# Kernel tuning notes

Hardware: AMD Instinct MI355X
Metric: run time of the kernel (lower is better)

The kernel has to match this reference:

```python
import jax, jax.numpy as jnp
import numpy as np

BATCH = 2048
N = 2 * BATCH
TEMP = 0.5
BN_EPS = 1e-5
COS_EPS = 1e-8

# Precompute (constant) flat indices of the negative entries: all (i,j) with
# j != i and j != i +- BATCH. Each row has exactly N-2 negatives.
_mask = np.ones((N, N), dtype=bool)
np.fill_diagonal(_mask, False)
for _i in range(BATCH):
    _mask[_i, BATCH + _i] = False
    _mask[BATCH + _i, _i] = False
NEG_IDX = np.nonzero(_mask.reshape(-1))[0]  # (N*(N-2),)


def _projector(h, W1, gamma, beta, W2, b2):
    # Linear (no bias) -> BatchNorm1d (training-mode batch stats) -> ReLU -> Linear
    x = h @ W1.T                                   # (B, latent)
    mu = jnp.mean(x, axis=0)
    var = jnp.mean(jnp.square(x - mu), axis=0)     # biased var, as torch BN
    x = (x - mu) * jax.lax.rsqrt(var + BN_EPS) * gamma + beta
    x = jax.nn.relu(x)
    return x @ W2.T + b2                           # (B, proj)


def setup_inputs() -> dict:
    key = jax.random.key(0)
    ks = jax.random.split(key, 4)
    latent, proj = 2048, 256
    return {
        "h_i": jax.random.normal(ks[0], (BATCH, latent), jnp.float32),
        "h_j": jax.random.normal(ks[1], (BATCH, latent), jnp.float32),
        "W1": jax.random.normal(ks[2], (latent, latent), jnp.float32) / np.sqrt(latent),
        "gamma": jnp.ones((latent,), jnp.float32),
        "beta": jnp.zeros((latent,), jnp.float32),
        "W2": jax.random.normal(ks[3], (proj, latent), jnp.float32) / np.sqrt(latent),
        "b2": jnp.zeros((proj,), jnp.float32),
    }


def reference(h_i, h_j, W1, gamma, beta, W2, b2):
    z_i = _projector(h_i, W1, gamma, beta, W2, b2)
    z_j = _projector(h_j, W1, gamma, beta, W2, b2)
    z = jnp.concatenate([z_i, z_j], axis=0)                      # (N, proj)
    # cosine similarity: normalize once, then a single GEMM
    zn = z / jnp.maximum(jnp.linalg.norm(z, axis=1, keepdims=True), COS_EPS)
    sim = (zn @ zn.T) / TEMP                                     # (N, N)
    sim_i_j = jnp.diagonal(sim, offset=BATCH)                    # (BATCH,)
    sim_j_i = jnp.diagonal(sim, offset=-BATCH)                   # (BATCH,)
    positives = jnp.concatenate([sim_i_j, sim_j_i])[:, None]     # (N, 1)
    negatives = sim.reshape(-1)[NEG_IDX].reshape(N, N - 2)       # (N, N-2)
    logits = jnp.concatenate([positives, negatives], axis=1)     # (N, N-1)
    # cross-entropy with label 0 for every row, reduction='sum', then / N
    loss = jnp.sum(jax.nn.logsumexp(logits, axis=1) - logits[:, 0]) / N
    return loss
```

## Files before the change

kernel.cpp:

```cpp
#include <hip/hip_runtime.h>
#include <math.h>

#define BATCH   2048
#define NROWS   4096
#define LATENT  2048
#define PROJ    256
#define TEMP_INV 2.0f
#define BN_EPS  1e-5f
#define COS_EPS 1e-8f

typedef __bf16 bf16x8 __attribute__((ext_vector_type(8)));
typedef float  f32x4  __attribute__((ext_vector_type(4)));

__device__ __forceinline__ unsigned short f2bf(float f) {
    union { float f; unsigned int u; } c; c.f = f;
    return (unsigned short)((c.u + 0x7FFFu + ((c.u >> 16) & 1u)) >> 16);
}
__device__ __forceinline__ float bf2f(unsigned short h) {
    union { unsigned int u; float f; } c; c.u = ((unsigned int)h) << 16;
    return c.f;
}

__device__ __forceinline__ void gl_lds16(const unsigned short* g, unsigned short* l) {
    __builtin_amdgcn_global_load_lds(
        (__attribute__((address_space(1))) void*)g,
        (__attribute__((address_space(3))) void*)l, 16, 0, 0);
}

#define G1 1048576
#define G2 2097152
#define G3 3145728
#define G4 3276800
__global__ __launch_bounds__(256) void cvt_all_kernel(
    const float* __restrict__ h_i, const float* __restrict__ h_j,
    const float* __restrict__ W1,  const float* __restrict__ W2,
    unsigned short* __restrict__ dst)
{
    int i = blockIdx.x * 256 + threadIdx.x;
    if (i >= G4) return;
    const float* src; int off;
    if (i < G1)      { src = h_i; off = i; }
    else if (i < G2) { src = h_j; off = i - G1; }
    else if (i < G3) { src = W1;  off = i - G2; }
    else             { src = W2;  off = i - G3; }
    float4 v = reinterpret_cast<const float4*>(src)[off];
    ushort4 o;
    o.x = f2bf(v.x); o.y = f2bf(v.y); o.z = f2bf(v.z); o.w = f2bf(v.w);
    reinterpret_cast<ushort4*>(dst)[i] = o;
}

template<int KSTRIDE, int KLEN, int WM, int WN>
__device__ __forceinline__ void mfma_loop(
    const unsigned short* __restrict__ Ab,
    const unsigned short* __restrict__ Bb,
    unsigned short* As, unsigned short* Bs,
    f32x4 acc[WM][WN], int tid)
{
    constexpr int BM = WM * 32;
    constexpr int BN = WN * 32;
    const int wid = tid >> 6, lane = tid & 63;
    const int mblk = (wid >> 1) * (WM * 16);
    const int nblk = (wid & 1) * (WN * 16);
    const int lr = lane & 15, lk = lane >> 4;
    for (int k0 = 0; k0 < KLEN; k0 += 32) {
        __syncthreads();
        #pragma unroll
        for (int u = 0; u < BM / 64; ++u) {
            int li = u * 256 + tid;
            gl_lds16(Ab + (size_t)(li >> 2) * KSTRIDE + k0 + (li & 3) * 8, As + li * 8);
        }
        #pragma unroll
        for (int u = 0; u < BN / 64; ++u) {
            int li = u * 256 + tid;
            gl_lds16(Bb + (size_t)(li >> 2) * KSTRIDE + k0 + (li & 3) * 8, Bs + li * 8);
        }
        __syncthreads();
        bf16x8 af[WM], bv[WN];
        #pragma unroll
        for (int i = 0; i < WM; ++i)
            af[i] = *reinterpret_cast<const bf16x8*>(As + (mblk + i * 16 + lr) * 32 + lk * 8);
        #pragma unroll
        for (int j = 0; j < WN; ++j)
            bv[j] = *reinterpret_cast<const bf16x8*>(Bs + (nblk + j * 16 + lr) * 32 + lk * 8);
        #pragma unroll
        for (int i = 0; i < WM; ++i)
            #pragma unroll
            for (int j = 0; j < WN; ++j)
                acc[i][j] = __builtin_amdgcn_mfma_f32_16x16x32_bf16(af[i], bv[j], acc[i][j], 0, 0, 0);
    }
}

__global__ __launch_bounds__(256) void gemm1_mfma(
    const unsigned short* __restrict__ Hb, const unsigned short* __restrict__ W1b,
    unsigned short* __restrict__ Xb, float* __restrict__ sums, float* __restrict__ sumsqs)
{
    __shared__ __align__(16) unsigned short As[64 * 32];
    __shared__ __align__(16) unsigned short Bs[128 * 32];
    const int tid = threadIdx.x;
    const int m0 = blockIdx.y * 64, n0 = blockIdx.x * 128;
    f32x4 zero = {0.f, 0.f, 0.f, 0.f};
    f32x4 acc[2][4];
    #pragma unroll
    for (int i = 0; i < 2; ++i)
        #pragma unroll
        for (int j = 0; j < 4; ++j) acc[i][j] = zero;
    mfma_loop<LATENT, LATENT, 2, 4>(Hb + (size_t)m0 * LATENT, W1b + (size_t)n0 * LATENT,
                                    As, Bs, acc, tid);
    const int wid = tid >> 6, lane = tid & 63;
    const int mblk = (wid >> 1) * 32, nblk = (wid & 1) * 64;
    const int lr = lane & 15, lq = lane >> 4;
    const int half = m0 >> 11;
    #pragma unroll
    for (int j = 0; j < 4; ++j) {
        float s = 0.f, q = 0.f;
        #pragma unroll
        for (int i = 0; i < 2; ++i)
            #pragma unroll
            for (int r = 0; r < 4; ++r) {
                float v = acc[i][j][r];
                s += v; q += v * v;
                int row = m0 + mblk + i * 16 + lq * 4 + r;
                int col = n0 + nblk + j * 16 + lr;
                Xb[(size_t)row * LATENT + col] = f2bf(v);
            }
        s += __shfl_xor(s, 16, 64);  q += __shfl_xor(q, 16, 64);
        s += __shfl_xor(s, 32, 64);  q += __shfl_xor(q, 32, 64);
        if (lq == 0) {
            int col = n0 + nblk + j * 16 + lr;
            atomicAdd(&sums[half * LATENT + col], s);
            atomicAdd(&sumsqs[half * LATENT + col], q);
        }
    }
}

__global__ __launch_bounds__(256) void bn_final_kernel(
    const float* __restrict__ sums, const float* __restrict__ sumsqs,
    const float* __restrict__ gamma, const float* __restrict__ beta,
    float* __restrict__ scaleA, float* __restrict__ shiftA)
{
    const int idx = blockIdx.x * 256 + threadIdx.x;
    const int c = idx & (LATENT - 1);
    float mu  = sums[idx] * (1.0f / BATCH);
    float var = sumsqs[idx] * (1.0f / BATCH) - mu * mu;
    float inv = rsqrtf(var + BN_EPS);
    float sc = gamma[c] * inv;
    scaleA[idx] = sc;
    shiftA[idx] = beta[c] - mu * sc;
}

__global__ __launch_bounds__(256) void bnrelu_kernel(
    unsigned short* __restrict__ Xb, const float* __restrict__ scaleA,
    const float* __restrict__ shiftA)
{
    int idx = (blockIdx.x * 256 + threadIdx.x) * 8;
    int row = idx >> 11;
    int col = idx & (LATENT - 1);
    int half = row >> 11;
    ushort4 a = *reinterpret_cast<const ushort4*>(Xb + idx);
    ushort4 b = *reinterpret_cast<const ushort4*>(Xb + idx + 4);
    float4 s0 = *reinterpret_cast<const float4*>(scaleA + half * LATENT + col);
    float4 s1 = *reinterpret_cast<const float4*>(scaleA + half * LATENT + col + 4);
    float4 h0 = *reinterpret_cast<const float4*>(shiftA + half * LATENT + col);
    float4 h1 = *reinterpret_cast<const float4*>(shiftA + half * LATENT + col + 4);
    ushort4 oa, ob;
    oa.x = f2bf(fmaxf(fmaf(bf2f(a.x), s0.x, h0.x), 0.f));
    oa.y = f2bf(fmaxf(fmaf(bf2f(a.y), s0.y, h0.y), 0.f));
    oa.z = f2bf(fmaxf(fmaf(bf2f(a.z), s0.z, h0.z), 0.f));
    oa.w = f2bf(fmaxf(fmaf(bf2f(a.w), s0.w, h0.w), 0.f));
    ob.x = f2bf(fmaxf(fmaf(bf2f(b.x), s1.x, h1.x), 0.f));
    ob.y = f2bf(fmaxf(fmaf(bf2f(b.y), s1.y, h1.y), 0.f));
    ob.z = f2bf(fmaxf(fmaf(bf2f(b.z), s1.z, h1.z), 0.f));
    ob.w = f2bf(fmaxf(fmaf(bf2f(b.w), s1.w, h1.w), 0.f));
    *reinterpret_cast<ushort4*>(Xb + idx) = oa;
    *reinterpret_cast<ushort4*>(Xb + idx + 4) = ob;
}

__global__ __launch_bounds__(256) void gemm2_mfma(
    const unsigned short* __restrict__ Xb, const unsigned short* __restrict__ W2b,
    float* __restrict__ Zp)
{
    __shared__ __align__(16) unsigned short As[128 * 32];
    __shared__ __align__(16) unsigned short Bs[64 * 32];
    const int tid = threadIdx.x;
    const int m0 = blockIdx.y * 128, n0 = blockIdx.x * 64, kc = blockIdx.z;
    f32x4 zero = {0.f, 0.f, 0.f, 0.f};
    f32x4 acc[4][2];
    #pragma unroll
    for (int i = 0; i < 4; ++i) { acc[i][0] = zero; acc[i][1] = zero; }
    mfma_loop<LATENT, 512, 4, 2>(Xb + (size_t)m0 * LATENT + kc * 512,
                                 W2b + (size_t)n0 * LATENT + kc * 512, As, Bs, acc, tid);
    float* Zk = Zp + (size_t)kc * NROWS * PROJ;
    const int wid = tid >> 6, lane = tid & 63;
    const int mblk = (wid >> 1) * 64, nblk = (wid & 1) * 32;
    const int lr = lane & 15, lq = lane >> 4;
    #pragma unroll
    for (int i = 0; i < 4; ++i)
        #pragma unroll
        for (int j = 0; j < 2; ++j)
            #pragma unroll
            for (int r = 0; r < 4; ++r) {
                int row = m0 + mblk + i * 16 + lq * 4 + r;
                int col = n0 + nblk + j * 16 + lr;
                Zk[(size_t)row * PROJ + col] = acc[i][j][r];
            }
}

__global__ __launch_bounds__(256) void rownorm_kernel(
    const float* __restrict__ Zp, const float* __restrict__ b2,
    unsigned short* __restrict__ ZNb)
{
    const int wave = threadIdx.x >> 6;
    const int lane = threadIdx.x & 63;
    const int row = blockIdx.x * 4 + wave;
    float v[4];
    float sq = 0.f;
    #pragma unroll
    for (int i = 0; i < 4; ++i) {
        int col = lane + i * 64;
        float t = b2[col];
        #pragma unroll
        for (int c = 0; c < 4; ++c)
            t += Zp[(size_t)c * NROWS * PROJ + (size_t)row * PROJ + col];
        v[i] = t;
        sq += t * t;
    }
    #pragma unroll
    for (int off = 32; off > 0; off >>= 1) sq += __shfl_xor(sq, off, 64);
    float inv = 1.0f / fmaxf(sqrtf(sq), COS_EPS);
    #pragma unroll
    for (int i = 0; i < 4; ++i)
        ZNb[(size_t)row * PROJ + lane + i * 64] = f2bf(v[i] * inv);
}

__global__ __launch_bounds__(256) void simlse_mfma(
    const unsigned short* __restrict__ ZNb, float* __restrict__ rowsum,
    float* __restrict__ dgA, float* __restrict__ posA)
{
    __shared__ __align__(16) unsigned short As[128 * 32];
    __shared__ __align__(16) unsigned short Bs[128 * 32];
    const int tid = threadIdx.x;
    const int r0 = blockIdx.y * 128, j0 = blockIdx.x * 128;
    f32x4 zero = {0.f, 0.f, 0.f, 0.f};
    f32x4 acc[4][4];
    #pragma unroll
    for (int i = 0; i < 4; ++i)
        #pragma unroll
        for (int j = 0; j < 4; ++j) acc[i][j] = zero;
    mfma_loop<PROJ, PROJ, 4, 4>(ZNb + (size_t)r0 * PROJ, ZNb + (size_t)j0 * PROJ,
                                As, Bs, acc, tid);
    const int wid = tid >> 6, lane = tid & 63;
    const int mblk = (wid >> 1) * 64, nblk = (wid & 1) * 64;
    const int lr = lane & 15, lq = lane >> 4;
    #pragma unroll
    for (int i = 0; i < 4; ++i)
        #pragma unroll
        for (int r = 0; r < 4; ++r) {
            int R = r0 + mblk + i * 16 + lq * 4 + r;
            int P = (R < BATCH) ? R + BATCH : R - BATCH;
            float t = 0.f;
            #pragma unroll
            for (int j = 0; j < 4; ++j) {
                int J = j0 + nblk + j * 16 + lr;
                float s = acc[i][j][r] * TEMP_INV;
                float e = __expf(s);
                t += e;
                if (J == R) dgA[R] = e;
                if (J == P) posA[R] = s;
            }
            t += __shfl_xor(t, 1, 64);
            t += __shfl_xor(t, 2, 64);
            t += __shfl_xor(t, 4, 64);
            t += __shfl_xor(t, 8, 64);
            if (lr == 0) atomicAdd(&rowsum[R], t);
        }
}

__global__ __launch_bounds__(256) void loss_kernel(
    const float* __restrict__ rowsum, const float* __restrict__ dgA,
    const float* __restrict__ posA, float* __restrict__ out)
{
    __shared__ float red[256];
    float s = 0.f;
    for (int r = threadIdx.x; r < NROWS; r += 256)
        s += logf(rowsum[r] - dgA[r]) - posA[r];
    red[threadIdx.x] = s;
    __syncthreads();
    for (int off = 128; off > 0; off >>= 1) {
        if (threadIdx.x < off) red[threadIdx.x] += red[threadIdx.x + off];
        __syncthreads();
    }
    if (threadIdx.x == 0) out[0] = red[0] * (1.0f / NROWS);
}

extern "C" void kernel_launch(void* const* d_in, const int* in_sizes, int n_in,
                              void* d_out, int out_size, void* d_ws, size_t ws_size,
                              hipStream_t stream)
{
    const float* h_i   = (const float*)d_in[0];
    const float* h_j   = (const float*)d_in[1];
    const float* W1    = (const float*)d_in[2];
    const float* gamma = (const float*)d_in[3];
    const float* beta  = (const float*)d_in[4];
    const float* W2    = (const float*)d_in[5];
    const float* b2    = (const float*)d_in[6];
    float* out = (float*)d_out;

    float* Zp     = (float*)d_ws;
    float* sums   = Zp + (size_t)4 * NROWS * PROJ;
    float* sumsqs = sums + 2 * LATENT;
    float* rowsum = sumsqs + 2 * LATENT;
    float* scaleA = rowsum + NROWS;
    float* shiftA = scaleA + 2 * LATENT;
    float* dgA    = shiftA + 2 * LATENT;
    float* posA   = dgA + NROWS;
    unsigned short* Hb  = (unsigned short*)(posA + NROWS);
    unsigned short* W1b = Hb + (size_t)NROWS * LATENT;
    unsigned short* W2b = W1b + (size_t)LATENT * LATENT;
    unsigned short* Xb  = W2b + (size_t)PROJ * LATENT;
    unsigned short* ZNb = Xb + (size_t)NROWS * LATENT;

    hipMemsetAsync(sums, 0, (size_t)(4 * LATENT + NROWS) * sizeof(float), stream);

    cvt_all_kernel<<<(G4 + 255) / 256, 256, 0, stream>>>(h_i, h_j, W1, W2, Hb);
    gemm1_mfma<<<dim3(LATENT / 128, NROWS / 64), 256, 0, stream>>>(Hb, W1b, Xb, sums, sumsqs);
    bn_final_kernel<<<(2 * LATENT) / 256, 256, 0, stream>>>(sums, sumsqs, gamma, beta, scaleA, shiftA);
    bnrelu_kernel<<<(NROWS * LATENT / 8) / 256, 256, 0, stream>>>(Xb, scaleA, shiftA);
    gemm2_mfma<<<dim3(PROJ / 64, NROWS / 128, 4), 256, 0, stream>>>(Xb, W2b, Zp);
    rownorm_kernel<<<NROWS / 4, 256, 0, stream>>>(Zp, b2, ZNb);
    simlse_mfma<<<dim3(NROWS / 128, NROWS / 128), 256, 0, stream>>>(ZNb, rowsum, dgA, posA);
    loss_kernel<<<1, 256, 0, stream>>>(rowsum, dgA, posA, out);
}
```

Before: 212.7 us.

## Use FP8 GEMM1, fuse BN+ReLU into GEMM2, swizzle LDS tiles

Inputs h and W1 are now quantized to FP8 e4m3, with W1 pre-scaled by 32. GEMM1 runs on fp8 MFMA with 128x128 tiles and a K-step of 128, and rescales the result in the epilogue. The standalone BN+ReLU pass is removed: GEMM2 applies scale, shift and ReLU to the A fragments after they come out of LDS. LDS layouts are also XOR-swizzled to cut bank conflicts. The main aim is to halve GEMM1 operand bytes and raise MFMA throughput, at the cost of FP8 quantization error in the projector's first layer.

Result: faster. 191.0 us (-10.2%).

```diff
diff --git a/kernel.cpp b/kernel.cpp
--- a/kernel.cpp
+++ b/kernel.cpp
@@ -1,4 +1,5 @@
 #include <hip/hip_runtime.h>
+#include <hip/hip_fp8.h>
 #include <math.h>
 
 #define BATCH   2048
@@ -8,9 +9,12 @@
 #define TEMP_INV 2.0f
 #define BN_EPS  1e-5f
 #define COS_EPS 1e-8f
+#define W1SCALE 32.0f
+#define W1INV   (1.0f / 32.0f)
 
 typedef __bf16 bf16x8 __attribute__((ext_vector_type(8)));
 typedef float  f32x4  __attribute__((ext_vector_type(4)));
+typedef long   i64;
 
 __device__ __forceinline__ unsigned short f2bf(float f) {
     union { float f; unsigned int u; } c; c.f = f;
@@ -20,11 +24,22 @@
     union { unsigned int u; float f; } c; c.u = ((unsigned int)h) << 16;
     return c.f;
 }
-
-__device__ __forceinline__ void gl_lds16(const unsigned short* g, unsigned short* l) {
+__device__ __forceinline__ unsigned char f2fp8(float f) {
+    __hip_fp8_e4m3 t(f);
+    return (unsigned char)t.__x;
+}
+
+__device__ __forceinline__ void gl_lds16(const void* g, void* l) {
     __builtin_amdgcn_global_load_lds(
-        (__attribute__((address_space(1))) void*)g,
+        (const __attribute__((address_space(1))) void*)g,
         (__attribute__((address_space(3))) void*)l, 16, 0, 0);
+}
+
+__device__ __forceinline__ int swz(int R, int lk) {
+    return R * 32 + ((lk ^ ((R >> 1) & 3)) << 3);
+}
+__device__ __forceinline__ int mix8(int R) {
+    return (R & 7) ^ ((R >> 1) & 4);
 }
 
 #define G1 1048576
@@ -34,19 +49,32 @@
 __global__ __launch_bounds__(256) void cvt_all_kernel(
     const float* __restrict__ h_i, const float* __restrict__ h_j,
     const float* __restrict__ W1,  const float* __restrict__ W2,
-    unsigned short* __restrict__ dst)
+    unsigned char* __restrict__ Hq, unsigned char* __restrict__ W1q,
+    unsigned short* __restrict__ W2b)
 {
     int i = blockIdx.x * 256 + threadIdx.x;
     if (i >= G4) return;
-    const float* src; int off;
-    if (i < G1)      { src = h_i; off = i; }
-    else if (i < G2) { src = h_j; off = i - G1; }
-    else if (i < G3) { src = W1;  off = i - G2; }
-    else             { src = W2;  off = i - G3; }
-    float4 v = reinterpret_cast<const float4*>(src)[off];
-    ushort4 o;
-    o.x = f2bf(v.x); o.y = f2bf(v.y); o.z = f2bf(v.z); o.w = f2bf(v.w);
-    reinterpret_cast<ushort4*>(dst)[i] = o;
+    if (i < G2) {
+        const float* src = (i < G1) ? h_i : h_j;
+        int off = (i < G1) ? i : i - G1;
+        float4 v = reinterpret_cast<const float4*>(src)[off];
+        uchar4 o;
+        o.x = f2fp8(v.x); o.y = f2fp8(v.y); o.z = f2fp8(v.z); o.w = f2fp8(v.w);
+        reinterpret_cast<uchar4*>(Hq)[i] = o;
+    } else if (i < G3) {
+        int off = i - G2;
+        float4 v = reinterpret_cast<const float4*>(W1)[off];
+        uchar4 o;
+        o.x = f2fp8(v.x * W1SCALE); o.y = f2fp8(v.y * W1SCALE);
+        o.z = f2fp8(v.z * W1SCALE); o.w = f2fp8(v.w * W1SCALE);
+        reinterpret_cast<uchar4*>(W1q)[off] = o;
+    } else {
+        int off = i - G3;
+        float4 v = reinterpret_cast<const float4*>(W2)[off];
+        ushort4 o;
+        o.x = f2bf(v.x); o.y = f2bf(v.y); o.z = f2bf(v.z); o.w = f2bf(v.w);
+        reinterpret_cast<ushort4*>(W2b)[off] = o;
+    }
 }
 
 template<int KSTRIDE, int KLEN, int WM, int WN>
@@ -67,21 +95,23 @@
         #pragma unroll
         for (int u = 0; u < BM / 64; ++u) {
             int li = u * 256 + tid;
-            gl_lds16(Ab + (size_t)(li >> 2) * KSTRIDE + k0 + (li & 3) * 8, As + li * 8);
+            int r = li >> 2, c = (li & 3) ^ ((li >> 3) & 3);
+            gl_lds16(Ab + (size_t)r * KSTRIDE + k0 + c * 8, As + li * 8);
         }
         #pragma unroll
         for (int u = 0; u < BN / 64; ++u) {
             int li = u * 256 + tid;
-            gl_lds16(Bb + (size_t)(li >> 2) * KSTRIDE + k0 + (li & 3) * 8, Bs + li * 8);
+            int r = li >> 2, c = (li & 3) ^ ((li >> 3) & 3);
+            gl_lds16(Bb + (size_t)r * KSTRIDE + k0 + c * 8, Bs + li * 8);
         }
         __syncthreads();
         bf16x8 af[WM], bv[WN];
         #pragma unroll
         for (int i = 0; i < WM; ++i)
-            af[i] = *reinterpret_cast<const bf16x8*>(As + (mblk + i * 16 + lr) * 32 + lk * 8);
+            af[i] = *reinterpret_cast<const bf16x8*>(As + swz(mblk + i * 16 + lr, lk));
         #pragma unroll
         for (int j = 0; j < WN; ++j)
-            bv[j] = *reinterpret_cast<const bf16x8*>(Bs + (nblk + j * 16 + lr) * 32 + lk * 8);
+            bv[j] = *reinterpret_cast<const bf16x8*>(Bs + swz(nblk + j * 16 + lr, lk));
         #pragma unroll
         for (int i = 0; i < WM; ++i)
             #pragma unroll
@@ -90,34 +120,86 @@
     }
 }
 
-__global__ __launch_bounds__(256) void gemm1_mfma(
-    const unsigned short* __restrict__ Hb, const unsigned short* __restrict__ W1b,
+__global__ __launch_bounds__(256) void gemm1_fp8(
+    const unsigned char* __restrict__ Hq, const unsigned char* __restrict__ W1q,
     unsigned short* __restrict__ Xb, float* __restrict__ sums, float* __restrict__ sumsqs)
 {
-    __shared__ __align__(16) unsigned short As[64 * 32];
-    __shared__ __align__(16) unsigned short Bs[128 * 32];
+    __shared__ __align__(16) unsigned char As[128 * 128];
+    __shared__ __align__(16) unsigned char Bs[128 * 128];
     const int tid = threadIdx.x;
-    const int m0 = blockIdx.y * 64, n0 = blockIdx.x * 128;
+    const int m0 = blockIdx.y * 128, n0 = blockIdx.x * 128;
+    const unsigned char* Ab = Hq + (size_t)m0 * LATENT;
+    const unsigned char* Bb = W1q + (size_t)n0 * LATENT;
+    const int wid = tid >> 6, lane = tid & 63;
+    const int mblk = (wid >> 1) * 64, nblk = (wid & 1) * 64;
+    const int lr = lane & 15, lk = lane >> 4;
     f32x4 zero = {0.f, 0.f, 0.f, 0.f};
-    f32x4 acc[2][4];
-    #pragma unroll
-    for (int i = 0; i < 2; ++i)
+    f32x4 acc[4][4];
+    #pragma unroll
+    for (int i = 0; i < 4; ++i)
         #pragma unroll
         for (int j = 0; j < 4; ++j) acc[i][j] = zero;
-    mfma_loop<LATENT, LATENT, 2, 4>(Hb + (size_t)m0 * LATENT, W1b + (size_t)n0 * LATENT,
-                                    As, Bs, acc, tid);
-    const int wid = tid >> 6, lane = tid & 63;
-    const int mblk = (wid >> 1) * 32, nblk = (wid & 1) * 64;
-    const int lr = lane & 15, lq = lane >> 4;
+
+    for (int k0 = 0; k0 < LATENT; k0 += 128) {
+        __syncthreads();
+        #pragma unroll
+        for (int u = 0; u < 4; ++u) {
+            int li = u * 256 + tid;
+            int r = li >> 3, s = li & 7;
+            int c = s ^ mix8(r);
+            gl_lds16(Ab + (size_t)r * LATENT + k0 + c * 16, As + li * 16);
+        }
+        #pragma unroll
+        for (int u = 0; u < 4; ++u) {
+            int li = u * 256 + tid;
+            int r = li >> 3, s = li & 7;
+            int c = s ^ mix8(r);
+            gl_lds16(Bb + (size_t)r * LATENT + k0 + c * 16, Bs + li * 16);
+        }
+        __syncthreads();
+        i64 af[4][4], bv[4][4];
+        #pragma unroll
+        for (int i = 0; i < 4; ++i) {
+            int R = mblk + i * 16 + lr;
+            int mr = mix8(R);
+            int base = R * 128 + (lk & 1) * 8;
+            #pragma unroll
+            for (int t = 0; t < 4; ++t) {
+                int g = 2 * t + (lk >> 1);
+                af[i][t] = *reinterpret_cast<const i64*>(As + base + ((g ^ mr) << 4));
+            }
+        }
+        #pragma unroll
+        for (int j = 0; j < 4; ++j) {
+            int R = nblk + j * 16 + lr;
+            int mr = mix8(R);
+            int base = R * 128 + (lk & 1) * 8;
+            #pragma unroll
+            for (int t = 0; t < 4; ++t) {
+                int g = 2 * t + (lk >> 1);
+                bv[j][t] = *reinterpret_cast<const i64*>(Bs + base + ((g ^ mr) << 4));
+            }
+        }
+        #pragma unroll
+        for (int t = 0; t < 4; ++t)
+            #pragma unroll
+            for (int i = 0; i < 4; ++i)
+                #pragma unroll
+                for (int j = 0; j < 4; ++j)
+                    acc[i][j] = __builtin_amdgcn_mfma_f32_16x16x32_fp8_fp8(
+                        af[i][t], bv[j][t], acc[i][j], 0, 0, 0);
+    }
+
+    const int lq = lane >> 4;
     const int half = m0 >> 11;
     #pragma unroll
     for (int j = 0; j < 4; ++j) {
         float s = 0.f, q = 0.f;
         #pragma unroll
-        for (int i = 0; i < 2; ++i)
+        for (int i = 0; i < 4; ++i)
             #pragma unroll
             for (int r = 0; r < 4; ++r) {
-                float v = acc[i][j][r];
+                float v = acc[i][j][r] * W1INV;
                 s += v; q += v * v;
                 int row = m0 + mblk + i * 16 + lq * 4 + r;
                 int col = n0 + nblk + j * 16 + lr;
@@ -148,51 +230,73 @@
     shiftA[idx] = beta[c] - mu * sc;
 }
 
-__global__ __launch_bounds__(256) void bnrelu_kernel(
-    unsigned short* __restrict__ Xb, const float* __restrict__ scaleA,
-    const float* __restrict__ shiftA)
-{
-    int idx = (blockIdx.x * 256 + threadIdx.x) * 8;
-    int row = idx >> 11;
-    int col = idx & (LATENT - 1);
-    int half = row >> 11;
-    ushort4 a = *reinterpret_cast<const ushort4*>(Xb + idx);
-    ushort4 b = *reinterpret_cast<const ushort4*>(Xb + idx + 4);
-    float4 s0 = *reinterpret_cast<const float4*>(scaleA + half * LATENT + col);
-    float4 s1 = *reinterpret_cast<const float4*>(scaleA + half * LATENT + col + 4);
-    float4 h0 = *reinterpret_cast<const float4*>(shiftA + half * LATENT + col);
-    float4 h1 = *reinterpret_cast<const float4*>(shiftA + half * LATENT + col + 4);
-    ushort4 oa, ob;
-    oa.x = f2bf(fmaxf(fmaf(bf2f(a.x), s0.x, h0.x), 0.f));
-    oa.y = f2bf(fmaxf(fmaf(bf2f(a.y), s0.y, h0.y), 0.f));
-    oa.z = f2bf(fmaxf(fmaf(bf2f(a.z), s0.z, h0.z), 0.f));
-    oa.w = f2bf(fmaxf(fmaf(bf2f(a.w), s0.w, h0.w), 0.f));
-    ob.x = f2bf(fmaxf(fmaf(bf2f(b.x), s1.x, h1.x), 0.f));
-    ob.y = f2bf(fmaxf(fmaf(bf2f(b.y), s1.y, h1.y), 0.f));
-    ob.z = f2bf(fmaxf(fmaf(bf2f(b.z), s1.z, h1.z), 0.f));
-    ob.w = f2bf(fmaxf(fmaf(bf2f(b.w), s1.w, h1.w), 0.f));
-    *reinterpret_cast<ushort4*>(Xb + idx) = oa;
-    *reinterpret_cast<ushort4*>(Xb + idx + 4) = ob;
-}
-
 __global__ __launch_bounds__(256) void gemm2_mfma(
     const unsigned short* __restrict__ Xb, const unsigned short* __restrict__ W2b,
+    const float* __restrict__ scaleA, const float* __restrict__ shiftA,
     float* __restrict__ Zp)
 {
     __shared__ __align__(16) unsigned short As[128 * 32];
     __shared__ __align__(16) unsigned short Bs[64 * 32];
     const int tid = threadIdx.x;
     const int m0 = blockIdx.y * 128, n0 = blockIdx.x * 64, kc = blockIdx.z;
+    const unsigned short* Ab = Xb + (size_t)m0 * LATENT + kc * 512;
+    const unsigned short* Bb = W2b + (size_t)n0 * LATENT + kc * 512;
+    const int half = m0 >> 11;
+    const float* scp = scaleA + half * LATENT + kc * 512;
+    const float* shp = shiftA + half * LATENT + kc * 512;
+    const int wid = tid >> 6, lane = tid & 63;
+    const int mblk = (wid >> 1) * 64, nblk = (wid & 1) * 32;
+    const int lr = lane & 15, lk = lane >> 4;
     f32x4 zero = {0.f, 0.f, 0.f, 0.f};
     f32x4 acc[4][2];
     #pragma unroll
     for (int i = 0; i < 4; ++i) { acc[i][0] = zero; acc[i][1] = zero; }
-    mfma_loop<LATENT, 512, 4, 2>(Xb + (size_t)m0 * LATENT + kc * 512,
-                                 W2b + (size_t)n0 * LATENT + kc * 512, As, Bs, acc, tid);
+
+    for (int k0 = 0; k0 < 512; k0 += 32) {
+        __syncthreads();
+        #pragma unroll
+        for (int u = 0; u < 2; ++u) {
+            int li = u * 256 + tid;
+            int r = li >> 2, c = (li & 3) ^ ((li >> 3) & 3);
+            gl_lds16(Ab + (size_t)r * LATENT + k0 + c * 8, As + li * 8);
+        }
+        {
+            int li = tid;
+            int r = li >> 2, c = (li & 3) ^ ((li >> 3) & 3);
+            gl_lds16(Bb + (size_t)r * LATENT + k0 + c * 8, Bs + li * 8);
+        }
+        __syncthreads();
+        float4 sc0 = *reinterpret_cast<const float4*>(scp + k0 + lk * 8);
+        float4 sc1 = *reinterpret_cast<const float4*>(scp + k0 + lk * 8 + 4);
+        float4 sh0 = *reinterpret_cast<const float4*>(shp + k0 + lk * 8);
+        float4 sh1 = *reinterpret_cast<const float4*>(shp + k0 + lk * 8 + 4);
+        bf16x8 af[4], bv[2];
+        #pragma unroll
+        for (int i = 0; i < 4; ++i) {
+            bf16x8 raw = *reinterpret_cast<const bf16x8*>(As + swz(mblk + i * 16 + lr, lk));
+            bf16x8 a;
+            a[0] = (__bf16)fmaxf(fmaf((float)raw[0], sc0.x, sh0.x), 0.f);
+            a[1] = (__bf16)fmaxf(fmaf((float)raw[1], sc0.y, sh0.y), 0.f);
+            a[2] = (__bf16)fmaxf(fmaf((float)raw[2], sc0.z, sh0.z), 0.f);
+            a[3] = (__bf16)fmaxf(fmaf((float)raw[3], sc0.w, sh0.w), 0.f);
+            a[4] = (__bf16)fmaxf(fmaf((float)raw[4], sc1.x, sh1.x), 0.f);
+            a[5] = (__bf16)fmaxf(fmaf((float)raw[5], sc1.y, sh1.y), 0.f);
+            a[6] = (__bf16)fmaxf(fmaf((float)raw[6], sc1.z, sh1.z), 0.f);
+            a[7] = (__bf16)fmaxf(fmaf((float)raw[7], sc1.w, sh1.w), 0.f);
+            af[i] = a;
+        }
+        #pragma unroll
+        for (int j = 0; j < 2; ++j)
+            bv[j] = *reinterpret_cast<const bf16x8*>(Bs + swz(nblk + j * 16 + lr, lk));
+        #pragma unroll
+        for (int i = 0; i < 4; ++i)
+            #pragma unroll
+            for (int j = 0; j < 2; ++j)
+                acc[i][j] = __builtin_amdgcn_mfma_f32_16x16x32_bf16(af[i], bv[j], acc[i][j], 0, 0, 0);
+    }
+
     float* Zk = Zp + (size_t)kc * NROWS * PROJ;
-    const int wid = tid >> 6, lane = tid & 63;
-    const int mblk = (wid >> 1) * 64, nblk = (wid & 1) * 32;
-    const int lr = lane & 15, lq = lane >> 4;
+    const int lq = lane >> 4;
     #pragma unroll
     for (int i = 0; i < 4; ++i)
         #pragma unroll
@@ -313,19 +417,18 @@
     float* shiftA = scaleA + 2 * LATENT;
     float* dgA    = shiftA + 2 * LATENT;
     float* posA   = dgA + NROWS;
-    unsigned short* Hb  = (unsigned short*)(posA + NROWS);
-    unsigned short* W1b = Hb + (size_t)NROWS * LATENT;
-    unsigned short* W2b = W1b + (size_t)LATENT * LATENT;
+    unsigned char* Hq  = (unsigned char*)(posA + NROWS);
+    unsigned char* W1q = Hq + (size_t)NROWS * LATENT;
+    unsigned short* W2b = (unsigned short*)(W1q + (size_t)LATENT * LATENT);
     unsigned short* Xb  = W2b + (size_t)PROJ * LATENT;
     unsigned short* ZNb = Xb + (size_t)NROWS * LATENT;
 
     hipMemsetAsync(sums, 0, (size_t)(4 * LATENT + NROWS) * sizeof(float), stream);
 
-    cvt_all_kernel<<<(G4 + 255) / 256, 256, 0, stream>>>(h_i, h_j, W1, W2, Hb);
-    gemm1_mfma<<<dim3(LATENT / 128, NROWS / 64), 256, 0, stream>>>(Hb, W1b, Xb, sums, sumsqs);
+    cvt_all_kernel<<<(G4 + 255) / 256, 256, 0, stream>>>(h_i, h_j, W1, W2, Hq, W1q, W2b);
+    gemm1_fp8<<<dim3(LATENT / 128, NROWS / 128), 256, 0, stream>>>(Hq, W1q, Xb, sums, sumsqs);
     bn_final_kernel<<<(2 * LATENT) / 256, 256, 0, stream>>>(sums, sumsqs, gamma, beta, scaleA, shiftA);
-    bnrelu_kernel<<<(NROWS * LATENT / 8) / 256, 256, 0, stream>>>(Xb, scaleA, shiftA);
-    gemm2_mfma<<<dim3(PROJ / 64, NROWS / 128, 4), 256, 0, stream>>>(Xb, W2b, Zp);
+    gemm2_mfma<<<dim3(PROJ / 64, NROWS / 128, 4), 256, 0, stream>>>(Xb, W2b, scaleA, shiftA, Zp);
     rownorm_kernel<<<NROWS / 4, 256, 0, stream>>>(Zp, b2, ZNb);
     simlse_mfma<<<dim3(NROWS / 128, NROWS / 128), 256, 0, stream>>>(ZNb, rowsum, dgA, posA);
     loss_kernel<<<1, 256, 0, stream>>>(rowsum, dgA, posA, out);
```
